# Kernel optimization log

Hardware: AMD Instinct MI355X
Metric: run time of the kernel (lower is better)

The kernel has to match this reference:

```python
import jax, jax.numpy as jnp
import numpy as np

# taxonomy level sizes: orders, families, genera, species
LEVEL_SIZES = [100, 400, 2000, 8000]
OFFSETS = [0, 100, 500, 2500]           # global-index offset of each level
N_TOTAL = 10500                          # sum of LEVEL_SIZES
B = 256
C = 8000                                 # max per-level class count (species)
NEG = -1e9


def _build_H():
    """Random but consistent hierarchy: each child node gets one parent; H[parent, child] = 1."""
    rng = np.random.default_rng(0)
    H = np.zeros((N_TOTAL, N_TOTAL), dtype=np.float32)
    for lvl in range(1, 4):
        n_child = LEVEL_SIZES[lvl]
        n_parent = LEVEL_SIZES[lvl - 1]
        parents = rng.integers(0, n_parent, size=n_child)
        H[OFFSETS[lvl - 1] + parents, OFFSETS[lvl] + np.arange(n_child)] = 1.0
    return jnp.asarray(H)


def setup_inputs() -> dict:
    key = jax.random.key(0)
    k1, k2 = jax.random.split(key)
    y_pred = jax.random.normal(k1, (B, 4, C), dtype=jnp.float32)
    # per-level targets in valid range
    cols = []
    for j in range(4):
        kj = jax.random.fold_in(k2, j)
        cols.append(jax.random.randint(kj, (B,), 0, LEVEL_SIZES[j]))
    y_true = jnp.stack(cols, axis=1).astype(jnp.int64)  # [B, 4]
    return {"y_pred": y_pred, "y_true": y_true, "H": _build_H()}


def reference(y_pred, y_true, H):
    weights = jnp.array([0.25, 0.25, 0.15, 0.1], dtype=y_pred.dtype)
    sizes = jnp.array(LEVEL_SIZES)                       # [4]
    offs = jnp.array(OFFSETS)                            # [4]

    # mask out invalid logits per level (levels have fewer classes than C)
    valid = jnp.arange(C)[None, :] < sizes[:, None]      # [4, C]
    logits = jnp.where(valid[None, :, :], y_pred, NEG)   # [B, 4, C]

    # per-level cross-entropy (mean over batch), vectorized over levels
    logp = jax.nn.log_softmax(logits, axis=-1)           # [B, 4, C]
    nll = -jnp.take_along_axis(logp, y_true[:, :, None], axis=2)[..., 0]  # [B, 4]
    ce = jnp.mean(nll, axis=0)                           # [4]

    # predicted global taxon indices per level
    g = jnp.argmax(logits, axis=-1) + offs[None, :]      # [B, 4]

    # parent-child consistency check via H gather: H[parent_pred, child_pred] == 1
    parent = g[:, :3]
    child = g[:, 1:]
    consistent = (H[parent, child] == 1.0).astype(y_pred.dtype)  # [B, 3]
    cons = jnp.float32(np.e) * jnp.sum(consistent, axis=0)       # [3]

    # loss = sum over levels j=1..3 of w[j] * (consistency_sum + CE_j)
    loss = jnp.sum(weights[1:] * (cons + ce[1:]))
    return loss
```

## Files before the change

### kernel.cpp

```cpp
#include <hip/hip_runtime.h>
#include <cmath>

#define C_DIM 8000
#define N_TOTAL 10500
#define B_DIM 256

__device__ __forceinline__ void merge_softmax_argmax(float& m, float& s, int& idx,
                                                     float m2, float s2, int i2) {
    if (m2 > m) {
        s = s * expf(m - m2) + s2;
        m = m2;
        idx = i2;
    } else if (m2 == m) {
        s += s2;
        if (i2 < idx) idx = i2;
    } else {
        s += s2 * expf(m2 - m);
    }
}

__global__ __launch_bounds__(256) void row_kernel(const float* __restrict__ yp,
                                                  const int* __restrict__ yt,
                                                  float* __restrict__ ws_nll,
                                                  int* __restrict__ ws_arg) {
    const int row = blockIdx.x;
    const int j = row & 3;
    const int tid = threadIdx.x;
    const int SIZES[4] = {100, 400, 2000, 8000};
    const int OFFS[4]  = {0, 100, 500, 2500};
    const int n = SIZES[j];
    const float* rowp = yp + (size_t)row * C_DIM;

    float m = -INFINITY, s = 0.0f;
    int idx = 0x7fffffff;
    for (int c = tid; c < n; c += 256) {
        float v = rowp[c];
        if (v > m) {
            s = s * expf(m - v) + 1.0f;
            m = v;
            idx = c;
        } else {
            s += expf(v - m);
        }
    }

    for (int off = 32; off; off >>= 1) {
        float m2 = __shfl_down(m, off, 64);
        float s2 = __shfl_down(s, off, 64);
        int   i2 = __shfl_down(idx, off, 64);
        merge_softmax_argmax(m, s, idx, m2, s2, i2);
    }

    __shared__ float sm[4], ss[4];
    __shared__ int si[4];
    const int wave = tid >> 6;
    if ((tid & 63) == 0) { sm[wave] = m; ss[wave] = s; si[wave] = idx; }
    __syncthreads();
    if (tid == 0) {
        for (int w = 1; w < 4; ++w) {
            merge_softmax_argmax(m, s, idx, sm[w], ss[w], si[w]);
        }
        const int t = yt[row];
        const float lse = m + logf(s);
        ws_nll[row] = -(rowp[t] - lse);
        ws_arg[row] = idx + OFFS[j];
    }
}

__global__ __launch_bounds__(256) void combine_kernel(const float* __restrict__ H,
                                                      const float* __restrict__ ws_nll,
                                                      const int* __restrict__ ws_arg,
                                                      float* __restrict__ out) {
    const int b = threadIdx.x;
    const float W1 = 0.25f, W2 = 0.15f, W3 = 0.10f;
    const float E = 2.718281828459045f;

    const int g0 = ws_arg[b * 4 + 0];
    const int g1 = ws_arg[b * 4 + 1];
    const int g2 = ws_arg[b * 4 + 2];
    const int g3 = ws_arg[b * 4 + 3];

    float p = 0.0f;
    p += W1 * (ws_nll[b * 4 + 1] * (1.0f / 256.0f));
    p += W2 * (ws_nll[b * 4 + 2] * (1.0f / 256.0f));
    p += W3 * (ws_nll[b * 4 + 3] * (1.0f / 256.0f));
    p += W1 * E * ((H[(size_t)g0 * N_TOTAL + g1] == 1.0f) ? 1.0f : 0.0f);
    p += W2 * E * ((H[(size_t)g1 * N_TOTAL + g2] == 1.0f) ? 1.0f : 0.0f);
    p += W3 * E * ((H[(size_t)g2 * N_TOTAL + g3] == 1.0f) ? 1.0f : 0.0f);

    for (int off = 32; off; off >>= 1) p += __shfl_down(p, off, 64);
    __shared__ float red[4];
    if ((b & 63) == 0) red[b >> 6] = p;
    __syncthreads();
    if (b == 0) out[0] = red[0] + red[1] + red[2] + red[3];
}

extern "C" void kernel_launch(void* const* d_in, const int* in_sizes, int n_in,
                              void* d_out, int out_size, void* d_ws, size_t ws_size,
                              hipStream_t stream) {
    const float* yp = (const float*)d_in[0];
    const int*   yt = (const int*)d_in[1];
    const float* H  = (const float*)d_in[2];

    float* ws_nll = (float*)d_ws;
    int*   ws_arg = (int*)((char*)d_ws + 1024 * sizeof(float));

    row_kernel<<<B_DIM * 4, 256, 0, stream>>>(yp, yt, ws_nll, ws_arg);
    combine_kernel<<<1, 256, 0, stream>>>(H, ws_nll, ws_arg, (float*)d_out);
}
```

Baseline: 499.5 us.

## Fuse combine into row kernel via last-block counter, vectorize loads, fast exp

Merges the per-row softmax/argmax kernel and the combine kernel into one launch, with the last finishing block (detected via an atomic counter and thread fences) doing the final reduction. Row loads become float4 and expf is replaced by __expf. This removes a kernel launch and a dependency gap but adds a memset launch and atomic/fence overhead, and slightly reduces exp precision.

```diff
diff --git a/kernel.cpp b/kernel.cpp
--- a/kernel.cpp
+++ b/kernel.cpp
@@ -4,25 +4,39 @@
 #define C_DIM 8000
 #define N_TOTAL 10500
 #define B_DIM 256
+#define N_ROWS (B_DIM * 4)
 
-__device__ __forceinline__ void merge_softmax_argmax(float& m, float& s, int& idx,
-                                                     float m2, float s2, int i2) {
+__device__ __forceinline__ void step(float& m, float& s, int& idx, float v, int c) {
+    if (v > m) {
+        s = s * __expf(m - v) + 1.0f;
+        m = v;
+        idx = c;
+    } else {
+        s += __expf(v - m);
+    }
+}
+
+__device__ __forceinline__ void merge_sa(float& m, float& s, int& idx,
+                                         float m2, float s2, int i2) {
     if (m2 > m) {
-        s = s * expf(m - m2) + s2;
+        s = s * __expf(m - m2) + s2;
         m = m2;
         idx = i2;
     } else if (m2 == m) {
         s += s2;
         if (i2 < idx) idx = i2;
     } else {
-        s += s2 * expf(m2 - m);
+        s += s2 * __expf(m2 - m);
     }
 }
 
-__global__ __launch_bounds__(256) void row_kernel(const float* __restrict__ yp,
-                                                  const int* __restrict__ yt,
-                                                  float* __restrict__ ws_nll,
-                                                  int* __restrict__ ws_arg) {
+__global__ __launch_bounds__(256) void fused_kernel(const float* __restrict__ yp,
+                                                    const int* __restrict__ yt,
+                                                    const float* __restrict__ H,
+                                                    int* __restrict__ counter,
+                                                    float* __restrict__ ws_nll,
+                                                    int* __restrict__ ws_arg,
+                                                    float* __restrict__ out) {
     const int row = blockIdx.x;
     const int j = row & 3;
     const int tid = threadIdx.x;
@@ -33,45 +47,46 @@
 
     float m = -INFINITY, s = 0.0f;
     int idx = 0x7fffffff;
-    for (int c = tid; c < n; c += 256) {
-        float v = rowp[c];
-        if (v > m) {
-            s = s * expf(m - v) + 1.0f;
-            m = v;
-            idx = c;
-        } else {
-            s += expf(v - m);
-        }
+    const float4* rowp4 = (const float4*)rowp;
+    const int n4 = n >> 2;
+    for (int c4 = tid; c4 < n4; c4 += 256) {
+        float4 v = rowp4[c4];
+        const int base = c4 << 2;
+        step(m, s, idx, v.x, base + 0);
+        step(m, s, idx, v.y, base + 1);
+        step(m, s, idx, v.z, base + 2);
+        step(m, s, idx, v.w, base + 3);
     }
 
     for (int off = 32; off; off >>= 1) {
         float m2 = __shfl_down(m, off, 64);
         float s2 = __shfl_down(s, off, 64);
         int   i2 = __shfl_down(idx, off, 64);
-        merge_softmax_argmax(m, s, idx, m2, s2, i2);
+        merge_sa(m, s, idx, m2, s2, i2);
     }
 
     __shared__ float sm[4], ss[4];
     __shared__ int si[4];
+    __shared__ float red[4];
+    __shared__ int isLast;
     const int wave = tid >> 6;
     if ((tid & 63) == 0) { sm[wave] = m; ss[wave] = s; si[wave] = idx; }
     __syncthreads();
     if (tid == 0) {
-        for (int w = 1; w < 4; ++w) {
-            merge_softmax_argmax(m, s, idx, sm[w], ss[w], si[w]);
-        }
+        m = sm[0]; s = ss[0]; idx = si[0];
+        for (int w = 1; w < 4; ++w) merge_sa(m, s, idx, sm[w], ss[w], si[w]);
         const int t = yt[row];
-        const float lse = m + logf(s);
-        ws_nll[row] = -(rowp[t] - lse);
+        ws_nll[row] = -(rowp[t] - (m + logf(s)));
         ws_arg[row] = idx + OFFS[j];
+        __threadfence();
+        int prev = atomicAdd(counter, 1);
+        isLast = (prev == N_ROWS - 1) ? 1 : 0;
     }
-}
+    __syncthreads();
+    if (!isLast) return;
 
-__global__ __launch_bounds__(256) void combine_kernel(const float* __restrict__ H,
-                                                      const float* __restrict__ ws_nll,
-                                                      const int* __restrict__ ws_arg,
-                                                      float* __restrict__ out) {
-    const int b = threadIdx.x;
+    __threadfence();
+    const int b = tid;
     const float W1 = 0.25f, W2 = 0.15f, W3 = 0.10f;
     const float E = 2.718281828459045f;
 
@@ -89,10 +104,9 @@
     p += W3 * E * ((H[(size_t)g2 * N_TOTAL + g3] == 1.0f) ? 1.0f : 0.0f);
 
     for (int off = 32; off; off >>= 1) p += __shfl_down(p, off, 64);
-    __shared__ float red[4];
-    if ((b & 63) == 0) red[b >> 6] = p;
+    if ((tid & 63) == 0) red[tid >> 6] = p;
     __syncthreads();
-    if (b == 0) out[0] = red[0] + red[1] + red[2] + red[3];
+    if (tid == 0) out[0] = red[0] + red[1] + red[2] + red[3];
 }
 
 extern "C" void kernel_launch(void* const* d_in, const int* in_sizes, int n_in,
@@ -102,9 +116,11 @@
     const int*   yt = (const int*)d_in[1];
     const float* H  = (const float*)d_in[2];
 
-    float* ws_nll = (float*)d_ws;
-    int*   ws_arg = (int*)((char*)d_ws + 1024 * sizeof(float));
+    int*   counter = (int*)d_ws;
+    float* ws_nll  = (float*)((char*)d_ws + 64);
+    int*   ws_arg  = (int*)((char*)d_ws + 64 + N_ROWS * sizeof(float));
 
-    row_kernel<<<B_DIM * 4, 256, 0, stream>>>(yp, yt, ws_nll, ws_arg);
-    combine_kernel<<<1, 256, 0, stream>>>(H, ws_nll, ws_arg, (float*)d_out);
+    hipMemsetAsync(counter, 0, sizeof(int), stream);
+    fused_kernel<<<N_ROWS, 256, 0, stream>>>(yp, yt, H, counter,
+                                             ws_nll, ws_arg, (float*)d_out);
 }
```

After: 505.7 us. Within noise of the previous version (+1.3%).
